# Performance work log

Measured on AMD Instinct MI355X. Metric: run time of the kernel, lower is better.

Reference implementation:

```python
import jax, jax.numpy as jnp
import numpy as np

NUM_USERS = 100000
NUM_ITEMS = 200000
D = 128          # embedding_dim
K = 4            # num interest heads
B = 4096
H = 256          # history length
H1, H2 = 512, 256  # hidden_units


def setup_inputs() -> dict:
    key = jax.random.key(0)
    ks = jax.random.split(key, 10)
    inp = {
        "user_ids": jax.random.randint(ks[0], (B,), 0, NUM_USERS),
        "candidate_items": jax.random.randint(ks[1], (B,), 0, NUM_ITEMS),
        "history_items": jax.random.randint(ks[2], (B, H), 0, NUM_ITEMS),
        "item_table": jax.random.normal(ks[3], (NUM_ITEMS, D), dtype=jnp.float32) * 0.05,
        "Wp": jax.random.normal(ks[4], (D, K), dtype=jnp.float32) * (1.0 / np.sqrt(D)),
        "W1": jax.random.normal(ks[5], (2 * D, H1), dtype=jnp.float32) * (1.0 / np.sqrt(2 * D)),
        "b1": jnp.zeros((H1,), dtype=jnp.float32),
        "W2": jax.random.normal(ks[6], (H1, H2), dtype=jnp.float32) * (1.0 / np.sqrt(H1)),
        "b2": jnp.zeros((H2,), dtype=jnp.float32),
        "W3": jax.random.normal(ks[7], (H2, 1), dtype=jnp.float32) * (1.0 / np.sqrt(H2)),
        "b3": jnp.zeros((1,), dtype=jnp.float32),
    }
    return inp


def reference(user_ids, candidate_items, history_items, item_table, Wp,
              W1, b1, W2, b2, W3, b3):
    # user_ids is unused by the original forward (user_emb never applied)
    item_vecs = item_table[history_items]          # (B, H, D)
    cand_vec = item_table[candidate_items]         # (B, D)

    # per-interest attention scores, softmax over history axis
    scores = jnp.einsum('bhd,dk->bhk', item_vecs, Wp)   # (B, H, K)
    scores = jax.nn.softmax(scores, axis=1)

    # softmax-weighted pooling -> K interest vectors per user
    interest_vectors = jnp.einsum('bhk,bhd->bkd', scores, item_vecs)  # (B, K, D)

    # similarity to candidate, pick best interest (data-dependent gather)
    sim_scores = jnp.einsum('bkd,bd->bk', interest_vectors, cand_vec)  # (B, K)
    best_idx = jnp.argmax(sim_scores, axis=-1)                          # (B,)
    selected = jnp.take_along_axis(
        interest_vectors, best_idx[:, None, None], axis=1)[:, 0, :]    # (B, D)

    # MLP tail: [2D -> 512] ReLU [512 -> 256] ReLU [256 -> 1], sigmoid
    x = jnp.concatenate([selected, cand_vec], axis=-1)  # (B, 2D)
    x = jax.nn.relu(x @ W1 + b1)
    x = jax.nn.relu(x @ W2 + b2)
    out = (x @ W3 + b3)[:, 0]                            # (B,)
    return jax.nn.sigmoid(out)
```

## Files before the change

### kernel.cpp

```cpp
#include <hip/hip_runtime.h>
#include <hip/hip_bf16.h>
#include <math.h>

#define B_SZ   4096
#define H_LEN  256
#define D_DIM  128
#define K_HEADS 4
#define H1_DIM 512
#define H2_DIM 256

#define CH     64
#define NCH    4
#define TPAD   132

__global__ __launch_bounds__(256, 4) void interest_kernel(
    const int*   __restrict__ cand_ids,
    const int*   __restrict__ hist,
    const float* __restrict__ table,
    const float* __restrict__ Wp,
    float*       __restrict__ X)
{
    __shared__ float tile[CH * TPAD];
    __shared__ float wpt[K_HEADS * D_DIM];
    __shared__ float exps4[CH * 4];
    __shared__ float candv[D_DIM];
    __shared__ int   rowids[H_LEN];
    __shared__ float lsumW[16];
    __shared__ float simred[4][K_HEADS];
    __shared__ int   bestk;

    const int b    = blockIdx.x;
    const int t    = threadIdx.x;
    const int lane = t & 63, w = t >> 6;
    const int r    = t >> 2, q = t & 3;
    const int d    = t & 127, half = t >> 7;

    if (t < D_DIM) {
        float4 w4 = ((const float4*)Wp)[t];
        wpt[0 * D_DIM + t] = w4.x;
        wpt[1 * D_DIM + t] = w4.y;
        wpt[2 * D_DIM + t] = w4.z;
        wpt[3 * D_DIM + t] = w4.w;
    }
    const int cand = cand_ids[b];
    if (t >= 128 && t < 160) {
        int c = t - 128;
        ((float4*)candv)[c] = ((const float4*)(table + (long long)cand * D_DIM))[c];
    }
    rowids[t] = hist[(long long)b * H_LEN + t];

    float a0 = 0.f, a1 = 0.f, a2 = 0.f, a3 = 0.f;
    float l0 = 0.f, l1 = 0.f, l2 = 0.f, l3 = 0.f;

    for (int c = 0; c < NCH; ++c) {
        __syncthreads();

        const int   row = rowids[(c << 6) + r];
        const float* rp = table + (long long)row * D_DIM + (q << 2);
        float4 v0 = *(const float4*)(rp + 0 * 16);
        float4 v1 = *(const float4*)(rp + 1 * 16);
        float4 v2 = *(const float4*)(rp + 2 * 16);
        float4 v3 = *(const float4*)(rp + 3 * 16);
        float4 v4 = *(const float4*)(rp + 4 * 16);
        float4 v5 = *(const float4*)(rp + 5 * 16);
        float4 v6 = *(const float4*)(rp + 6 * 16);
        float4 v7 = *(const float4*)(rp + 7 * 16);

        float s0 = 0.f, s1 = 0.f, s2 = 0.f, s3 = 0.f;
        float4 va;
        #define DO_J(J, VV)                                                     \
        {   va = VV;                                                            \
            const int cb = (q << 2) + (J << 4);                                 \
            float4 w0 = *(const float4*)(wpt + 0 * D_DIM + cb);                 \
            float4 w1 = *(const float4*)(wpt + 1 * D_DIM + cb);                 \
            float4 w2 = *(const float4*)(wpt + 2 * D_DIM + cb);                 \
            float4 w3 = *(const float4*)(wpt + 3 * D_DIM + cb);                 \
            s0 += va.x * w0.x + va.y * w0.y + va.z * w0.z + va.w * w0.w;        \
            s1 += va.x * w1.x + va.y * w1.y + va.z * w1.z + va.w * w1.w;        \
            s2 += va.x * w2.x + va.y * w2.y + va.z * w2.z + va.w * w2.w;        \
            s3 += va.x * w3.x + va.y * w3.y + va.z * w3.z + va.w * w3.w;        \
            *(float4*)(tile + r * TPAD + cb) = va;                              \
        }
        DO_J(0, v0) DO_J(1, v1) DO_J(2, v2) DO_J(3, v3)
        DO_J(4, v4) DO_J(5, v5) DO_J(6, v6) DO_J(7, v7)
        #undef DO_J

        s0 += __shfl_xor(s0, 1); s0 += __shfl_xor(s0, 2);
        s1 += __shfl_xor(s1, 1); s1 += __shfl_xor(s1, 2);
        s2 += __shfl_xor(s2, 1); s2 += __shfl_xor(s2, 2);
        s3 += __shfl_xor(s3, 1); s3 += __shfl_xor(s3, 2);

        float e0 = expf(s0), e1 = expf(s1), e2 = expf(s2), e3 = expf(s3);
        if (q == 0) ((float4*)exps4)[r] = make_float4(e0, e1, e2, e3);

        float t0 = e0, t1 = e1, t2 = e2, t3 = e3;
        #pragma unroll
        for (int off = 4; off <= 32; off <<= 1) {
            t0 += __shfl_xor(t0, off);
            t1 += __shfl_xor(t1, off);
            t2 += __shfl_xor(t2, off);
            t3 += __shfl_xor(t3, off);
        }
        l0 += t0; l1 += t1; l2 += t2; l3 += t3;

        __syncthreads();

        #pragma unroll 8
        for (int i = 0; i < 32; ++i) {
            int hl = (half << 5) + i;
            float4 e4 = ((const float4*)exps4)[hl];
            float  vv = tile[hl * TPAD + d];
            a0 += e4.x * vv; a1 += e4.y * vv; a2 += e4.z * vv; a3 += e4.w * vv;
        }
    }

    __syncthreads();
    float* partBp = tile;
    float* ivbufp = tile + 512;

    if (half == 1) ((float4*)partBp)[d] = make_float4(a0, a1, a2, a3);
    if (lane == 0) ((float4*)lsumW)[w]  = make_float4(l0, l1, l2, l3);
    __syncthreads();

    float s0 = 0.f, s1 = 0.f, s2 = 0.f, s3 = 0.f;
    if (half == 0) {
        float4 pb = ((const float4*)partBp)[d];
        float4 L0 = ((const float4*)lsumW)[0];
        float4 L1 = ((const float4*)lsumW)[1];
        float4 L2 = ((const float4*)lsumW)[2];
        float4 L3 = ((const float4*)lsumW)[3];
        float i0 = 1.f / (L0.x + L1.x + L2.x + L3.x);
        float i1 = 1.f / (L0.y + L1.y + L2.y + L3.y);
        float i2 = 1.f / (L0.z + L1.z + L2.z + L3.z);
        float i3 = 1.f / (L0.w + L1.w + L2.w + L3.w);
        a0 = (a0 + pb.x) * i0;
        a1 = (a1 + pb.y) * i1;
        a2 = (a2 + pb.z) * i2;
        a3 = (a3 + pb.w) * i3;
        ((float4*)ivbufp)[d] = make_float4(a0, a1, a2, a3);
        float cd = candv[d];
        s0 = a0 * cd; s1 = a1 * cd; s2 = a2 * cd; s3 = a3 * cd;
    }
    #pragma unroll
    for (int off = 32; off >= 1; off >>= 1) {
        s0 += __shfl_xor(s0, off);
        s1 += __shfl_xor(s1, off);
        s2 += __shfl_xor(s2, off);
        s3 += __shfl_xor(s3, off);
    }
    if (lane == 0) {
        simred[w][0] = s0; simred[w][1] = s1;
        simred[w][2] = s2; simred[w][3] = s3;
    }
    __syncthreads();

    if (t == 0) {
        float sim[4];
        #pragma unroll
        for (int k = 0; k < 4; ++k)
            sim[k] = simred[0][k] + simred[1][k] + simred[2][k] + simred[3][k];
        int best = 0;
        #pragma unroll
        for (int k = 1; k < 4; ++k) if (sim[k] > sim[best]) best = k;
        bestk = best;
    }
    __syncthreads();

    float* xrow = X + (long long)b * (2 * D_DIM);
    if (t < 128) xrow[t] = ivbufp[t * 4 + bestk];
    else         xrow[t] = candv[t - 128];
}

#define GT  64
#define GBK 32

__global__ __launch_bounds__(256) void gemm_bias_relu(
    const float* __restrict__ A, const float* __restrict__ W,
    const float* __restrict__ bias, float* __restrict__ C,
    int M, int N, int K)
{
    __shared__ float As[GBK * GT];
    __shared__ float Ws[GBK * GT];
    const int t  = threadIdx.x;
    const int tx = t & 15, ty = t >> 4;
    const int n0 = blockIdx.x * GT, m0 = blockIdx.y * GT;

    float acc[4][4] = {{0.f}};

    const int am = t >> 2, aq = t & 3;
    const int wk = t >> 3, wr = t & 7;

    for (int k0 = 0; k0 < K; k0 += GBK) {
        float4 fa0 = *(const float4*)(A + (long long)(m0 + am) * K + k0 + aq * 8);
        float4 fa1 = *(const float4*)(A + (long long)(m0 + am) * K + k0 + aq * 8 + 4);
        float4 fw0 = *(const float4*)(W + (long long)(k0 + wk) * N + n0 + wr * 8);
        float4 fw1 = *(const float4*)(W + (long long)(k0 + wk) * N + n0 + wr * 8 + 4);
        __syncthreads();
        As[(aq * 8 + 0) * GT + am] = fa0.x;
        As[(aq * 8 + 1) * GT + am] = fa0.y;
        As[(aq * 8 + 2) * GT + am] = fa0.z;
        As[(aq * 8 + 3) * GT + am] = fa0.w;
        As[(aq * 8 + 4) * GT + am] = fa1.x;
        As[(aq * 8 + 5) * GT + am] = fa1.y;
        As[(aq * 8 + 6) * GT + am] = fa1.z;
        As[(aq * 8 + 7) * GT + am] = fa1.w;
        *(float4*)(Ws + wk * GT + wr * 8)     = fw0;
        *(float4*)(Ws + wk * GT + wr * 8 + 4) = fw1;
        __syncthreads();
        #pragma unroll
        for (int kk = 0; kk < GBK; ++kk) {
            float4 a4 = *(const float4*)(As + kk * GT + ty * 4);
            float4 w4 = *(const float4*)(Ws + kk * GT + tx * 4);
            acc[0][0] += a4.x * w4.x; acc[0][1] += a4.x * w4.y;
            acc[0][2] += a4.x * w4.z; acc[0][3] += a4.x * w4.w;
            acc[1][0] += a4.y * w4.x; acc[1][1] += a4.y * w4.y;
            acc[1][2] += a4.y * w4.z; acc[1][3] += a4.y * w4.w;
            acc[2][0] += a4.z * w4.x; acc[2][1] += a4.z * w4.y;
            acc[2][2] += a4.z * w4.z; acc[2][3] += a4.z * w4.w;
            acc[3][0] += a4.w * w4.x; acc[3][1] += a4.w * w4.y;
            acc[3][2] += a4.w * w4.z; acc[3][3] += a4.w * w4.w;
        }
    }

    float4 bv = *(const float4*)(bias + n0 + tx * 4);
    #pragma unroll
    for (int i = 0; i < 4; ++i) {
        float4 c;
        c.x = fmaxf(acc[i][0] + bv.x, 0.f);
        c.y = fmaxf(acc[i][1] + bv.y, 0.f);
        c.z = fmaxf(acc[i][2] + bv.z, 0.f);
        c.w = fmaxf(acc[i][3] + bv.w, 0.f);
        *(float4*)(C + (long long)(m0 + ty * 4 + i) * N + n0 + tx * 4) = c;
    }
}

__global__ __launch_bounds__(256) void head_kernel(
    const float* __restrict__ H2buf,
    const float* __restrict__ W3,
    const float* __restrict__ b3,
    float*       __restrict__ out)
{
    const int b = blockIdx.x * 256 + threadIdx.x;
    const float4* hp = (const float4*)(H2buf + (long long)b * H2_DIM);
    const float4* wp = (const float4*)W3;
    float acc = 0.f;
    #pragma unroll 8
    for (int i = 0; i < H2_DIM / 4; ++i) {
        float4 h = hp[i], wv = wp[i];
        acc += h.x * wv.x + h.y * wv.y + h.z * wv.z + h.w * wv.w;
    }
    float z = acc + b3[0];
    out[b] = 1.f / (1.f + expf(-z));
}

extern "C" void kernel_launch(void* const* d_in, const int* in_sizes, int n_in,
                              void* d_out, int out_size, void* d_ws, size_t ws_size,
                              hipStream_t stream) {
    const int*   cand  = (const int*)  d_in[1];
    const int*   hist  = (const int*)  d_in[2];
    const float* table = (const float*)d_in[3];
    const float* Wp    = (const float*)d_in[4];
    const float* W1    = (const float*)d_in[5];
    const float* b1    = (const float*)d_in[6];
    const float* W2    = (const float*)d_in[7];
    const float* b2    = (const float*)d_in[8];
    const float* W3    = (const float*)d_in[9];
    const float* b3    = (const float*)d_in[10];
    float* out = (float*)d_out;

    float* X   = (float*)d_ws;
    float* Hc1 = X   + (size_t)B_SZ * 2 * D_DIM;
    float* Hc2 = Hc1 + (size_t)B_SZ * H1_DIM;

    interest_kernel<<<B_SZ, 256, 0, stream>>>(cand, hist, table, Wp, X);
    gemm_bias_relu<<<dim3(H1_DIM / GT, B_SZ / GT), 256, 0, stream>>>(
        X, W1, b1, Hc1, B_SZ, H1_DIM, 2 * D_DIM);
    gemm_bias_relu<<<dim3(H2_DIM / GT, B_SZ / GT), 256, 0, stream>>>(
        Hc1, W2, b2, Hc2, B_SZ, H2_DIM, H1_DIM);
    head_kernel<<<B_SZ / 256, 256, 0, stream>>>(Hc2, W3, b3, out);
}
```

Before: 288.9 us.

## Run MLP layers on bf16 MFMA with pre-transposed bf16 weights

```diff
diff --git a/kernel.cpp b/kernel.cpp
--- a/kernel.cpp
+++ b/kernel.cpp
@@ -13,12 +13,15 @@
 #define NCH    4
 #define TPAD   132
 
+typedef __attribute__((ext_vector_type(8))) short bf16x8;
+typedef __attribute__((ext_vector_type(4))) float f32x4;
+
 __global__ __launch_bounds__(256, 4) void interest_kernel(
     const int*   __restrict__ cand_ids,
     const int*   __restrict__ hist,
     const float* __restrict__ table,
     const float* __restrict__ Wp,
-    float*       __restrict__ X)
+    __hip_bfloat16* __restrict__ Xbf)
 {
     __shared__ float tile[CH * TPAD];
     __shared__ float wpt[K_HEADS * D_DIM];
@@ -166,71 +169,65 @@
     }
     __syncthreads();
 
-    float* xrow = X + (long long)b * (2 * D_DIM);
-    if (t < 128) xrow[t] = ivbufp[t * 4 + bestk];
-    else         xrow[t] = candv[t - 128];
-}
-
-#define GT  64
-#define GBK 32
-
-__global__ __launch_bounds__(256) void gemm_bias_relu(
-    const float* __restrict__ A, const float* __restrict__ W,
-    const float* __restrict__ bias, float* __restrict__ C,
-    int M, int N, int K)
-{
-    __shared__ float As[GBK * GT];
-    __shared__ float Ws[GBK * GT];
-    const int t  = threadIdx.x;
-    const int tx = t & 15, ty = t >> 4;
-    const int n0 = blockIdx.x * GT, m0 = blockIdx.y * GT;
-
-    float acc[4][4] = {{0.f}};
-
-    const int am = t >> 2, aq = t & 3;
-    const int wk = t >> 3, wr = t & 7;
-
-    for (int k0 = 0; k0 < K; k0 += GBK) {
-        float4 fa0 = *(const float4*)(A + (long long)(m0 + am) * K + k0 + aq * 8);
-        float4 fa1 = *(const float4*)(A + (long long)(m0 + am) * K + k0 + aq * 8 + 4);
-        float4 fw0 = *(const float4*)(W + (long long)(k0 + wk) * N + n0 + wr * 8);
-        float4 fw1 = *(const float4*)(W + (long long)(k0 + wk) * N + n0 + wr * 8 + 4);
-        __syncthreads();
-        As[(aq * 8 + 0) * GT + am] = fa0.x;
-        As[(aq * 8 + 1) * GT + am] = fa0.y;
-        As[(aq * 8 + 2) * GT + am] = fa0.z;
-        As[(aq * 8 + 3) * GT + am] = fa0.w;
-        As[(aq * 8 + 4) * GT + am] = fa1.x;
-        As[(aq * 8 + 5) * GT + am] = fa1.y;
-        As[(aq * 8 + 6) * GT + am] = fa1.z;
-        As[(aq * 8 + 7) * GT + am] = fa1.w;
-        *(float4*)(Ws + wk * GT + wr * 8)     = fw0;
-        *(float4*)(Ws + wk * GT + wr * 8 + 4) = fw1;
-        __syncthreads();
-        #pragma unroll
-        for (int kk = 0; kk < GBK; ++kk) {
-            float4 a4 = *(const float4*)(As + kk * GT + ty * 4);
-            float4 w4 = *(const float4*)(Ws + kk * GT + tx * 4);
-            acc[0][0] += a4.x * w4.x; acc[0][1] += a4.x * w4.y;
-            acc[0][2] += a4.x * w4.z; acc[0][3] += a4.x * w4.w;
-            acc[1][0] += a4.y * w4.x; acc[1][1] += a4.y * w4.y;
-            acc[1][2] += a4.y * w4.z; acc[1][3] += a4.y * w4.w;
-            acc[2][0] += a4.z * w4.x; acc[2][1] += a4.z * w4.y;
-            acc[2][2] += a4.z * w4.z; acc[2][3] += a4.z * w4.w;
-            acc[3][0] += a4.w * w4.x; acc[3][1] += a4.w * w4.y;
-            acc[3][2] += a4.w * w4.z; acc[3][3] += a4.w * w4.w;
-        }
-    }
-
-    float4 bv = *(const float4*)(bias + n0 + tx * 4);
+    __hip_bfloat16* xrow = Xbf + (long long)b * (2 * D_DIM);
+    if (t < 128) xrow[t] = __float2bfloat16(ivbufp[t * 4 + bestk]);
+    else         xrow[t] = __float2bfloat16(candv[t - 128]);
+}
+
+__global__ __launch_bounds__(256) void convert_weights(
+    const float* __restrict__ W1, const float* __restrict__ W2,
+    __hip_bfloat16* __restrict__ W1t, __hip_bfloat16* __restrict__ W2t)
+{
+    int idx = blockIdx.x * 256 + threadIdx.x;
+    if (idx < 2 * D_DIM * H1_DIM) {
+        int n = idx >> 8, k = idx & 255;
+        W1t[idx] = __float2bfloat16(W1[k * H1_DIM + n]);
+    } else {
+        int j = idx - 2 * D_DIM * H1_DIM;
+        int n = j >> 9, k = j & 511;
+        W2t[j] = __float2bfloat16(W2[k * H2_DIM + n]);
+    }
+}
+
+template<int N, int K, bool OUT_BF16>
+__global__ __launch_bounds__(256) void mfma_mlp(
+    const __hip_bfloat16* __restrict__ A,
+    const __hip_bfloat16* __restrict__ Bt,
+    const float* __restrict__ bias,
+    void* __restrict__ Cout)
+{
+    const int t    = threadIdx.x;
+    const int wave = t >> 6, lane = t & 63;
+    const int lm   = lane & 15, quad = lane >> 4;
+    const int n0   = blockIdx.x * 16;
+    const int m0   = blockIdx.y * 64 + wave * 16;
+
+    const __hip_bfloat16* Ap = A  + (long long)(m0 + lm) * K + quad * 8;
+    const __hip_bfloat16* Bp = Bt + (long long)(n0 + lm) * K + quad * 8;
+
+    f32x4 acc = {0.f, 0.f, 0.f, 0.f};
+    for (int kc = 0; kc < K; kc += 256) {
+        bf16x8 af[8], bfr[8];
+        #pragma unroll
+        for (int it = 0; it < 8; ++it) {
+            af[it]  = *(const bf16x8*)(Ap + kc + it * 32);
+            bfr[it] = *(const bf16x8*)(Bp + kc + it * 32);
+        }
+        #pragma unroll
+        for (int it = 0; it < 8; ++it)
+            acc = __builtin_amdgcn_mfma_f32_16x16x32_bf16(af[it], bfr[it], acc, 0, 0, 0);
+    }
+
+    const int n  = n0 + lm;
+    const float bv = bias[n];
     #pragma unroll
     for (int i = 0; i < 4; ++i) {
-        float4 c;
-        c.x = fmaxf(acc[i][0] + bv.x, 0.f);
-        c.y = fmaxf(acc[i][1] + bv.y, 0.f);
-        c.z = fmaxf(acc[i][2] + bv.z, 0.f);
-        c.w = fmaxf(acc[i][3] + bv.w, 0.f);
-        *(float4*)(C + (long long)(m0 + ty * 4 + i) * N + n0 + tx * 4) = c;
+        int m = m0 + quad * 4 + i;
+        float v = fmaxf(acc[i] + bv, 0.f);
+        if (OUT_BF16)
+            ((__hip_bfloat16*)Cout)[(long long)m * N + n] = __float2bfloat16(v);
+        else
+            ((float*)Cout)[(long long)m * N + n] = v;
     }
 }
 
@@ -268,14 +265,19 @@
     const float* b3    = (const float*)d_in[10];
     float* out = (float*)d_out;
 
-    float* X   = (float*)d_ws;
-    float* Hc1 = X   + (size_t)B_SZ * 2 * D_DIM;
-    float* Hc2 = Hc1 + (size_t)B_SZ * H1_DIM;
-
-    interest_kernel<<<B_SZ, 256, 0, stream>>>(cand, hist, table, Wp, X);
-    gemm_bias_relu<<<dim3(H1_DIM / GT, B_SZ / GT), 256, 0, stream>>>(
-        X, W1, b1, Hc1, B_SZ, H1_DIM, 2 * D_DIM);
-    gemm_bias_relu<<<dim3(H2_DIM / GT, B_SZ / GT), 256, 0, stream>>>(
-        Hc1, W2, b2, Hc2, B_SZ, H2_DIM, H1_DIM);
+    char* p = (char*)d_ws;
+    __hip_bfloat16* Xbf  = (__hip_bfloat16*)p;                  p += (size_t)B_SZ * 2 * D_DIM * 2;
+    __hip_bfloat16* Hc1  = (__hip_bfloat16*)p;                  p += (size_t)B_SZ * H1_DIM * 2;
+    float*          Hc2  = (float*)p;                           p += (size_t)B_SZ * H2_DIM * 4;
+    __hip_bfloat16* W1t  = (__hip_bfloat16*)p;                  p += (size_t)H1_DIM * 2 * D_DIM * 2;
+    __hip_bfloat16* W2t  = (__hip_bfloat16*)p;
+
+    convert_weights<<<(2 * D_DIM * H1_DIM + H1_DIM * H2_DIM) / 256, 256, 0, stream>>>(
+        W1, W2, W1t, W2t);
+    interest_kernel<<<B_SZ, 256, 0, stream>>>(cand, hist, table, Wp, Xbf);
+    mfma_mlp<H1_DIM, 2 * D_DIM, true><<<dim3(H1_DIM / 16, B_SZ / 64), 256, 0, stream>>>(
+        Xbf, W1t, b1, Hc1);
+    mfma_mlp<H2_DIM, H1_DIM, false><<<dim3(H2_DIM / 16, B_SZ / 64), 256, 0, stream>>>(
+        Hc1, W2t, b2, Hc2);
     head_kernel<<<B_SZ / 256, 256, 0, stream>>>(Hc2, W3, b3, out);
 }
```

New measurement: 274.8 us. 1.05x faster.
